# Optimization experiments

Measured on AMD Instinct MI355X. Metric: run time of the kernel, lower is better.

## Reference

```python
import jax, jax.numpy as jnp
import numpy as np

N_NODES = 50000
N_EDGES = 800000
NFEAT = 256
NHID = 128
NCLASS = 40
NLAYERS = 3


def setup_inputs() -> dict:
    key = jax.random.key(0)
    ks = jax.random.split(key, 8)
    x = jax.random.normal(ks[0], (N_NODES, NFEAT), dtype=jnp.float32)
    edge_src = jax.random.randint(ks[1], (N_EDGES,), 0, N_NODES, dtype=jnp.int32)
    edge_dst = jax.random.randint(ks[2], (N_EDGES,), 0, N_NODES, dtype=jnp.int32)
    # Kaiming-ish scaled params
    W_in = jax.random.normal(ks[3], (NFEAT, NHID), dtype=jnp.float32) / np.sqrt(NFEAT)
    b_in = jnp.zeros((NHID,), dtype=jnp.float32)
    W_mlps = jax.random.normal(ks[4], (NLAYERS, NHID, NHID), dtype=jnp.float32) / np.sqrt(NHID)
    b_mlps = jnp.zeros((NLAYERS, NHID), dtype=jnp.float32)
    W_out = jax.random.normal(ks[5], (NHID, NCLASS), dtype=jnp.float32) / np.sqrt(NHID)
    b_out = jnp.zeros((NCLASS,), dtype=jnp.float32)
    return {"x": x, "edge_src": edge_src, "edge_dst": edge_dst,
            "W_in": W_in, "b_in": b_in, "W_mlps": W_mlps, "b_mlps": b_mlps,
            "W_out": W_out, "b_out": b_out}


def reference(x, edge_src, edge_dst, W_in, b_in, W_mlps, b_mlps, W_out, b_out):
    # Dropout is identity in eval mode (training=False).
    n = x.shape[0]
    h = jax.nn.relu(x @ W_in + b_in)                       # [N, H]
    for i in range(NLAYERS):
        # GINConv with eps=0: h' = h + sum_{(s->d) in E} h[s] scattered to d
        agg = jax.ops.segment_sum(h[edge_src], edge_dst, num_segments=n)
        h = jax.nn.relu((h + agg) @ W_mlps[i] + b_mlps[i])  # [N, H]
    logits = h @ W_out + b_out                              # [N, C]
    return jax.nn.log_softmax(logits, axis=1)
```

## Files before the change

kernel.cpp:

```cpp
#include <hip/hip_runtime.h>
#include <math.h>

#define NHID 128
#define NFEAT 256
#define NCLASS 40

typedef __bf16 bf16x8 __attribute__((ext_vector_type(8)));
typedef __bf16 bf16x4 __attribute__((ext_vector_type(4)));
typedef float floatx4 __attribute__((ext_vector_type(4)));


__global__ __launch_bounds__(256) void bucket_hist(const int* __restrict__ edst,
                                                   int* __restrict__ bucket_counts,
                                                   int E, int nbuck) {
    __shared__ int lh[256];
    int tid = threadIdx.x;
    lh[tid] = 0;
    __syncthreads();
    int base = blockIdx.x * 4096;
#pragma unroll
    for (int k = 0; k < 16; ++k) {
        int e = base + k * 256 + tid;
        if (e < E) atomicAdd(&lh[edst[e] >> 8], 1);
    }
    __syncthreads();
    if (tid < nbuck && lh[tid]) atomicAdd(&bucket_counts[tid], lh[tid]);
}

__global__ __launch_bounds__(256) void bucket_scan(const int* __restrict__ counts,
                                                   int* __restrict__ start,
                                                   int* __restrict__ cursor,
                                                   int* __restrict__ row_ptr,
                                                   int nbuck, int E, int N) {
    __shared__ int lds[256];
    int tid = threadIdx.x;
    int v = (tid < nbuck) ? counts[tid] : 0;
    lds[tid] = v;
    __syncthreads();
    for (int off = 1; off < 256; off <<= 1) {
        int t = (tid >= off) ? lds[tid - off] : 0;
        __syncthreads();
        lds[tid] += t;
        __syncthreads();
    }
    int excl = lds[tid] - v;
    if (tid < nbuck) { start[tid] = excl; cursor[tid] = excl; }
    if (tid == 0) { start[nbuck] = E; row_ptr[N] = E; }
}

__global__ __launch_bounds__(256) void bucket_scatter(const int* __restrict__ esrc,
                                                      const int* __restrict__ edst,
                                                      int* __restrict__ cursor,
                                                      unsigned int* __restrict__ bdata,
                                                      int E, int nbuck) {
    __shared__ int lh[256];
    __shared__ int lbase[256];
    int tid = threadIdx.x;
    lh[tid] = 0;
    __syncthreads();
    int base = blockIdx.x * 4096;
    unsigned int recs[16];
    short bks[16];
    short lofs[16];
#pragma unroll
    for (int k = 0; k < 16; ++k) {
        int e = base + k * 256 + tid;
        bks[k] = -1;
        if (e < E) {
            int d = edst[e];
            int s = esrc[e];
            int b = d >> 8;
            recs[k] = ((unsigned int)(d & 255) << 16) | (unsigned int)s;
            bks[k] = (short)b;
            lofs[k] = (short)atomicAdd(&lh[b], 1);
        }
    }
    __syncthreads();
    if (tid < nbuck && lh[tid]) lbase[tid] = atomicAdd(&cursor[tid], lh[tid]);
    __syncthreads();
#pragma unroll
    for (int k = 0; k < 16; ++k) {
        if (bks[k] >= 0) bdata[lbase[bks[k]] + lofs[k]] = recs[k];
    }
}

__global__ __launch_bounds__(256) void bucket_finalize(const unsigned int* __restrict__ bdata,
                                                       const int* __restrict__ start,
                                                       int* __restrict__ row_ptr,
                                                       int* __restrict__ srcs,
                                                       int N) {
    __shared__ int hist[256];
    __shared__ int cur[256];
    int b = blockIdx.x;
    int tid = threadIdx.x;
    int s0 = start[b];
    int cnt = start[b + 1] - s0;
    hist[tid] = 0;
    __syncthreads();
    for (int i = tid; i < cnt; i += 256) atomicAdd(&hist[bdata[s0 + i] >> 16], 1);
    __syncthreads();
    int v0 = hist[tid];
    __syncthreads();
    for (int off = 1; off < 256; off <<= 1) {
        int t = (tid >= off) ? hist[tid - off] : 0;
        __syncthreads();
        hist[tid] += t;
        __syncthreads();
    }
    int excl = hist[tid] - v0;
    cur[tid] = excl;
    int node = b * 256 + tid;
    if (node < N) row_ptr[node] = s0 + excl;
    __syncthreads();
    for (int i = tid; i < cnt; i += 256) {
        unsigned int r = bdata[s0 + i];
        int p = atomicAdd(&cur[r >> 16], 1);
        srcs[s0 + p] = (int)(r & 0xffffu);
    }
}

template <int K>
__global__ __launch_bounds__(256) void transpose_split(const float* __restrict__ src,
                                                       __bf16* __restrict__ dhi,
                                                       __bf16* __restrict__ dlo, int total) {
    int i = blockIdx.x * 256 + threadIdx.x;
    if (i >= total) return;
    int per = 128 * K;
    int l = i / per;
    int r = i - l * per;
    int n = r / K;
    int k = r - n * K;
    float v = src[(size_t)l * per + (size_t)k * 128 + n];
    __bf16 hi = (__bf16)v;
    dhi[i] = hi;
    dlo[i] = (__bf16)(v - (float)hi);
}

__global__ __launch_bounds__(256) void aggregate_fused(const __bf16* __restrict__ hhi,
                                                       const __bf16* __restrict__ hlo,
                                                       const int* __restrict__ row_ptr,
                                                       const int* __restrict__ srcs,
                                                       __bf16* __restrict__ ohi,
                                                       __bf16* __restrict__ olo, int N) {
    int tid = threadIdx.x;
    int node = blockIdx.x * 4 + (tid >> 6);
    if (node >= N) return;
    int lane = tid & 63;
    int g = lane >> 4;
    int c = lane & 15;
    int beg = row_ptr[node];
    int end = row_ptr[node + 1];
    const bf16x8* hv = (const bf16x8*)hhi;

    float a[8], b2[8];
#pragma unroll
    for (int j = 0; j < 8; ++j) { a[j] = 0.f; b2[j] = 0.f; }

    int i = beg;
    for (; i + 8 <= end; i += 8) {
        int s0 = srcs[i + g];
        int s1 = srcs[i + 4 + g];
        bf16x8 v0 = hv[(size_t)s0 * 16 + c];
        bf16x8 v1 = hv[(size_t)s1 * 16 + c];
#pragma unroll
        for (int j = 0; j < 8; ++j) { a[j] += (float)v0[j]; b2[j] += (float)v1[j]; }
    }
    for (; i < end; i += 4) {
        if (i + g < end) {
            int s = srcs[i + g];
            bf16x8 v = hv[(size_t)s * 16 + c];
#pragma unroll
            for (int j = 0; j < 8; ++j) a[j] += (float)v[j];
        }
    }
#pragma unroll
    for (int j = 0; j < 8; ++j) a[j] += b2[j];
#pragma unroll
    for (int j = 0; j < 8; ++j) a[j] += __shfl_xor(a[j], 16);
#pragma unroll
    for (int j = 0; j < 8; ++j) a[j] += __shfl_xor(a[j], 32);

    if (g == 0) {
        bf16x8 sh = ((const bf16x8*)hhi)[(size_t)node * 16 + c];
        bf16x8 sl = ((const bf16x8*)hlo)[(size_t)node * 16 + c];
        bf16x8 whi, wlo;
#pragma unroll
        for (int j = 0; j < 8; ++j) {
            float v = a[j] + (float)sh[j] + (float)sl[j];
            __bf16 h = (__bf16)v;
            whi[j] = h;
            wlo[j] = (__bf16)(v - (float)h);
        }
        ((bf16x8*)ohi)[(size_t)node * 16 + c] = whi;
        ((bf16x8*)olo)[(size_t)node * 16 + c] = wlo;
    }
}

template <int MODE>
__global__ __launch_bounds__(256) void gemm_mfma(
    const float* __restrict__ Af, const __bf16* __restrict__ Ahi,
    const __bf16* __restrict__ Alo,
    const __bf16* __restrict__ Wthi, const __bf16* __restrict__ Wtlo,
    const float* __restrict__ bias, __bf16* __restrict__ Ohi,
    __bf16* __restrict__ Olo, int M, int K) {
    __shared__ __align__(16) char smem[49152];
    __bf16* sAhi = (__bf16*)smem;
    __bf16* sAlo = (__bf16*)(smem + 8192);
    __bf16* sWhi = (__bf16*)(smem + 16384);
    __bf16* sWlo = (__bf16*)(smem + 32768);

    int tid = threadIdx.x;
    int row0 = blockIdx.x * 64;
    int wave = tid >> 6;
    int l = tid & 63;
    int m16 = l & 15;
    int q = l >> 4;
    int axor = m16 & 7;
    int arow = wave * 16 + m16;

    floatx4 acc[8];
#pragma unroll
    for (int t = 0; t < 8; ++t) acc[t] = (floatx4){0.f, 0.f, 0.f, 0.f};

    for (int k0 = 0; k0 < K; k0 += 64) {
#pragma unroll
        for (int it = 0; it < 2; ++it) {
            int lin = it * 2048 + tid * 8;
            int row = lin >> 6, k = lin & 63;
            int g = min(row0 + row, M - 1);
            int off = row * 64 + (((k >> 3) ^ (row & 7)) << 3);
            if (MODE == 0) {
                float4 v0 = *(const float4*)&Af[(size_t)g * K + k0 + k];
                float4 v1 = *(const float4*)&Af[(size_t)g * K + k0 + k + 4];
                float s[8] = {v0.x, v0.y, v0.z, v0.w, v1.x, v1.y, v1.z, v1.w};
                bf16x8 shi, slo;
#pragma unroll
                for (int j = 0; j < 8; ++j) {
                    __bf16 h = (__bf16)s[j];
                    shi[j] = h;
                    slo[j] = (__bf16)(s[j] - (float)h);
                }
                *(bf16x8*)(sAhi + off) = shi;
                *(bf16x8*)(sAlo + off) = slo;
            } else {
                *(bf16x8*)(sAhi + off) = *(const bf16x8*)&Ahi[(size_t)g * 128 + k0 + k];
                *(bf16x8*)(sAlo + off) = *(const bf16x8*)&Alo[(size_t)g * 128 + k0 + k];
            }
        }
#pragma unroll
        for (int it = 0; it < 4; ++it) {
            int lin = it * 2048 + tid * 8;
            int n = lin >> 6, kk = lin & 63;
            int off = n * 64 + (((kk >> 3) ^ (n & 7)) << 3);
            *(bf16x8*)(sWhi + off) = *(const bf16x8*)&Wthi[(size_t)n * K + k0 + kk];
            *(bf16x8*)(sWlo + off) = *(const bf16x8*)&Wtlo[(size_t)n * K + k0 + kk];
        }
        __syncthreads();

#pragma unroll
        for (int s = 0; s < 2; ++s) {
            int sw = (((s * 4 + q) ^ axor) << 3);
            bf16x8 ahi = *(bf16x8*)(sAhi + arow * 64 + sw);
            bf16x8 alo = *(bf16x8*)(sAlo + arow * 64 + sw);
#pragma unroll
            for (int t = 0; t < 8; ++t) {
                int n = t * 16 + m16;
                bf16x8 bhi = *(bf16x8*)(sWhi + n * 64 + sw);
                bf16x8 blo = *(bf16x8*)(sWlo + n * 64 + sw);
                acc[t] = __builtin_amdgcn_mfma_f32_16x16x32_bf16(ahi, bhi, acc[t], 0, 0, 0);
                acc[t] = __builtin_amdgcn_mfma_f32_16x16x32_bf16(alo, bhi, acc[t], 0, 0, 0);
                acc[t] = __builtin_amdgcn_mfma_f32_16x16x32_bf16(ahi, blo, acc[t], 0, 0, 0);
            }
        }
        __syncthreads();
    }

    float* eps = (float*)(smem + 16384);
#pragma unroll
    for (int t = 0; t < 8; ++t) {
        int col = t * 16 + m16;
        float bb = bias[col];
#pragma unroll
        for (int i = 0; i < 4; ++i) {
            int row = wave * 16 + q * 4 + i;
            eps[row * 128 + col] = fmaxf(acc[t][i] + bb, 0.f);
        }
    }
    __syncthreads();
#pragma unroll
    for (int it = 0; it < 8; ++it) {
        int lin = it * 1024 + tid * 4;
        int row = lin >> 7, col = lin & 127;
        int g = row0 + row;
        if (g < M) {
            float4 v = *(float4*)(eps + lin);
            bf16x4 hi, lo;
            float vv[4] = {v.x, v.y, v.z, v.w};
#pragma unroll
            for (int j = 0; j < 4; ++j) {
                __bf16 h = (__bf16)vv[j];
                hi[j] = h;
                lo[j] = (__bf16)(vv[j] - (float)h);
            }
            *(bf16x4*)&Ohi[(size_t)g * 128 + col] = hi;
            *(bf16x4*)&Olo[(size_t)g * 128 + col] = lo;
        }
    }
}

__global__ __launch_bounds__(256) void out_logsoftmax(const __bf16* __restrict__ hhi,
                                                      const __bf16* __restrict__ hlo,
                                                      const float* __restrict__ Wout,
                                                      const float* __restrict__ bout,
                                                      float* __restrict__ out, int M) {
    __shared__ float sW[128 * NCLASS];
    __shared__ float sb[NCLASS];
    __shared__ float sH[32 * 132];
    int tid = threadIdx.x;
    for (int i = tid; i < 128 * NCLASS; i += 256) sW[i] = Wout[i];
    if (tid < NCLASS) sb[tid] = bout[tid];
    int row0 = blockIdx.x * 32;
#pragma unroll
    for (int it = 0; it < 4; ++it) {
        int i = tid * 4 + it * 1024;
        int r = i >> 7, k = i & 127;
        int rr = min(row0 + r, M - 1);
        uint2 uh = *(const uint2*)&hhi[(size_t)rr * 128 + k];
        uint2 ul = *(const uint2*)&hlo[(size_t)rr * 128 + k];
        sH[r * 132 + k + 0] = __uint_as_float(uh.x << 16) + __uint_as_float(ul.x << 16);
        sH[r * 132 + k + 1] = __uint_as_float(uh.x & 0xffff0000u) + __uint_as_float(ul.x & 0xffff0000u);
        sH[r * 132 + k + 2] = __uint_as_float(uh.y << 16) + __uint_as_float(ul.y << 16);
        sH[r * 132 + k + 3] = __uint_as_float(uh.y & 0xffff0000u) + __uint_as_float(ul.y & 0xffff0000u);
    }
    __syncthreads();

    int r = tid >> 3;
    int cg = tid & 7;
    float z[5];
#pragma unroll
    for (int j = 0; j < 5; ++j) z[j] = sb[cg * 5 + j];
    for (int k = 0; k < 128; ++k) {
        float a = sH[r * 132 + k];
#pragma unroll
        for (int j = 0; j < 5; ++j) z[j] += a * sW[k * NCLASS + cg * 5 + j];
    }
    float m = z[0];
#pragma unroll
    for (int j = 1; j < 5; ++j) m = fmaxf(m, z[j]);
    for (int off = 1; off < 8; off <<= 1) m = fmaxf(m, __shfl_xor(m, off));
    float s = 0.f;
#pragma unroll
    for (int j = 0; j < 5; ++j) s += expf(z[j] - m);
    for (int off = 1; off < 8; off <<= 1) s += __shfl_xor(s, off);
    float lse = m + logf(s);
    int row = row0 + r;
    if (row < M) {
#pragma unroll
        for (int j = 0; j < 5; ++j) out[(size_t)row * NCLASS + cg * 5 + j] = z[j] - lse;
    }
}

extern "C" void kernel_launch(void* const* d_in, const int* in_sizes, int n_in,
                              void* d_out, int out_size, void* d_ws, size_t ws_size,
                              hipStream_t stream) {
    const float* x      = (const float*)d_in[0];
    const int*   esrc   = (const int*)d_in[1];
    const int*   edst   = (const int*)d_in[2];
    const float* W_in   = (const float*)d_in[3];
    const float* b_in   = (const float*)d_in[4];
    const float* W_mlps = (const float*)d_in[5];
    const float* b_mlps = (const float*)d_in[6];
    const float* W_out  = (const float*)d_in[7];
    const float* b_out  = (const float*)d_in[8];
    float* out = (float*)d_out;

    int N = in_sizes[0] / NFEAT;
    int E = in_sizes[1];
    int nbuck = (N + 255) >> 8;

    char* ws = (char*)d_ws;
    size_t hb = (((size_t)N * NHID * sizeof(__bf16)) + 255) & ~(size_t)255;
    __bf16* h_hi_a = (__bf16*)ws;
    __bf16* h_lo_a = (__bf16*)(ws + hb);
    __bf16* h_hi_b = (__bf16*)(ws + 2 * hb);
    __bf16* h_lo_b = (__bf16*)(ws + 3 * hb);
    __bf16* sum_hi = (__bf16*)(ws + 4 * hb);
    __bf16* sum_lo = (__bf16*)(ws + 5 * hb);
    unsigned int* bdata = (unsigned int*)(ws + 4 * hb);
    char* ip = ws + 6 * hb;
    int* row_ptr = (int*)ip;  ip += (((size_t)(N + 1) * 4) + 255) & ~(size_t)255;
    int* srcs    = (int*)ip;  ip += (((size_t)E * 4) + 255) & ~(size_t)255;
    int* bucket_counts = (int*)ip;  ip += 1024;
    int* bucket_start  = (int*)ip;  ip += 1024;
    int* bucket_cursor = (int*)ip;  ip += 1024;
    __bf16* Wt_in_hi   = (__bf16*)ip;  ip += 128 * NFEAT * 2;
    __bf16* Wt_in_lo   = (__bf16*)ip;  ip += 128 * NFEAT * 2;
    __bf16* Wt_mlps_hi = (__bf16*)ip;  ip += 3 * 128 * NHID * 2;
    __bf16* Wt_mlps_lo = (__bf16*)ip;  ip += 3 * 128 * NHID * 2;

    int eb4 = (E + 4095) / 4096;

    hipMemsetAsync(bucket_counts, 0, 1024, stream);
    bucket_hist<<<eb4, 256, 0, stream>>>(edst, bucket_counts, E, nbuck);
    bucket_scan<<<1, 256, 0, stream>>>(bucket_counts, bucket_start, bucket_cursor,
                                       row_ptr, nbuck, E, N);
    bucket_scatter<<<eb4, 256, 0, stream>>>(esrc, edst, bucket_cursor, bdata, E, nbuck);
    bucket_finalize<<<nbuck, 256, 0, stream>>>(bdata, bucket_start, row_ptr, srcs, N);

    transpose_split<NFEAT><<<(128 * NFEAT + 255) / 256, 256, 0, stream>>>(
        W_in, Wt_in_hi, Wt_in_lo, 128 * NFEAT);
    transpose_split<NHID><<<(3 * 128 * NHID + 255) / 256, 256, 0, stream>>>(
        W_mlps, Wt_mlps_hi, Wt_mlps_lo, 3 * 128 * NHID);

    int gb = (N + 63) / 64;
    gemm_mfma<0><<<gb, 256, 0, stream>>>(x, (const __bf16*)nullptr, (const __bf16*)nullptr,
                                         Wt_in_hi, Wt_in_lo, b_in, h_hi_a, h_lo_a, N, NFEAT);

    __bf16* cur_hi = h_hi_a; __bf16* cur_lo = h_lo_a;
    __bf16* nxt_hi = h_hi_b; __bf16* nxt_lo = h_lo_b;
    for (int i = 0; i < 3; ++i) {
        aggregate_fused<<<(N + 3) / 4, 256, 0, stream>>>(cur_hi, cur_lo, row_ptr, srcs,
                                                         sum_hi, sum_lo, N);
        gemm_mfma<1><<<gb, 256, 0, stream>>>(
            (const float*)nullptr, sum_hi, sum_lo,
            Wt_mlps_hi + (size_t)i * 128 * NHID, Wt_mlps_lo + (size_t)i * 128 * NHID,
            b_mlps + (size_t)i * NHID, nxt_hi, nxt_lo, N, NHID);
        __bf16* t;
        t = cur_hi; cur_hi = nxt_hi; nxt_hi = t;
        t = cur_lo; cur_lo = nxt_lo; nxt_lo = t;
    }

    out_logsoftmax<<<(N + 31) / 32, 256, 0, stream>>>(cur_hi, cur_lo, W_out, b_out, out, N);
}
```

Before: 327.9 us.

## Split hidden features into quarter-planes for cache-friendly neighbour aggregation

The GEMM epilogue and the output kernel now store and read hidden activations in four column-quarter planes of 32 features each. Aggregation walks one quarter at a time over a contiguous node range per block, so the gathered working set per pass is a quarter of the full feature matrix and is more likely to stay in cache. The aggregate kernel also changes to a persistent grid of 1024 blocks with 16 nodes per wave and 4 lanes per node, and uses non-temporal loads and stores. Costs are that the edge list and row pointers are read four times, lanes are less parallel per node, and the aggregate output stays row-major while the GEMM reads it as before.

```diff
diff --git a/kernel.cpp b/kernel.cpp
--- a/kernel.cpp
+++ b/kernel.cpp
@@ -136,63 +136,71 @@
     dlo[i] = (__bf16)(v - (float)hi);
 }
 
-__global__ __launch_bounds__(256) void aggregate_fused(const __bf16* __restrict__ hhi,
-                                                       const __bf16* __restrict__ hlo,
-                                                       const int* __restrict__ row_ptr,
-                                                       const int* __restrict__ srcs,
-                                                       __bf16* __restrict__ ohi,
-                                                       __bf16* __restrict__ olo, int N) {
-    int tid = threadIdx.x;
-    int node = blockIdx.x * 4 + (tid >> 6);
-    if (node >= N) return;
+__global__ __launch_bounds__(256) void aggregate_q(const __bf16* __restrict__ hhi,
+                                                   const __bf16* __restrict__ hlo,
+                                                   const int* __restrict__ row_ptr,
+                                                   const int* __restrict__ srcs,
+                                                   __bf16* __restrict__ ohi,
+                                                   __bf16* __restrict__ olo, int N) {
+    int tid = threadIdx.x;
+    int wave = tid >> 6;
     int lane = tid & 63;
-    int g = lane >> 4;
-    int c = lane & 15;
-    int beg = row_ptr[node];
-    int end = row_ptr[node + 1];
-    const bf16x8* hv = (const bf16x8*)hhi;
-
-    float a[8], b2[8];
-#pragma unroll
-    for (int j = 0; j < 8; ++j) { a[j] = 0.f; b2[j] = 0.f; }
-
-    int i = beg;
-    for (; i + 8 <= end; i += 8) {
-        int s0 = srcs[i + g];
-        int s1 = srcs[i + 4 + g];
-        bf16x8 v0 = hv[(size_t)s0 * 16 + c];
-        bf16x8 v1 = hv[(size_t)s1 * 16 + c];
-#pragma unroll
-        for (int j = 0; j < 8; ++j) { a[j] += (float)v0[j]; b2[j] += (float)v1[j]; }
-    }
-    for (; i < end; i += 4) {
-        if (i + g < end) {
-            int s = srcs[i + g];
-            bf16x8 v = hv[(size_t)s * 16 + c];
-#pragma unroll
-            for (int j = 0; j < 8; ++j) a[j] += (float)v[j];
-        }
-    }
-#pragma unroll
-    for (int j = 0; j < 8; ++j) a[j] += b2[j];
-#pragma unroll
-    for (int j = 0; j < 8; ++j) a[j] += __shfl_xor(a[j], 16);
-#pragma unroll
-    for (int j = 0; j < 8; ++j) a[j] += __shfl_xor(a[j], 32);
-
-    if (g == 0) {
-        bf16x8 sh = ((const bf16x8*)hhi)[(size_t)node * 16 + c];
-        bf16x8 sl = ((const bf16x8*)hlo)[(size_t)node * 16 + c];
-        bf16x8 whi, wlo;
-#pragma unroll
-        for (int j = 0; j < 8; ++j) {
-            float v = a[j] + (float)sh[j] + (float)sl[j];
-            __bf16 h = (__bf16)v;
-            whi[j] = h;
-            wlo[j] = (__bf16)(v - (float)h);
-        }
-        ((bf16x8*)ohi)[(size_t)node * 16 + c] = whi;
-        ((bf16x8*)olo)[(size_t)node * 16 + c] = wlo;
+    int nsub = lane >> 2;
+    int c = lane & 3;
+    int per = (N + (int)gridDim.x - 1) / (int)gridDim.x;
+    int nb = (int)blockIdx.x * per;
+    int ne = nb + per;
+    if (ne > N) ne = N;
+    size_t qstride = (size_t)N * 32;
+    for (int q = 0; q < 4; ++q) {
+        const bf16x8* hq = (const bf16x8*)(hhi + (size_t)q * qstride);
+        const bf16x8* lq = (const bf16x8*)(hlo + (size_t)q * qstride);
+        for (int n0 = nb + wave * 16; n0 < ne; n0 += 64) {
+            int node = n0 + nsub;
+            bool valid = node < ne;
+            int beg = 0, end = 0;
+            if (valid) {
+                beg = row_ptr[node];
+                end = row_ptr[node + 1];
+            }
+            float a[8];
+#pragma unroll
+            for (int j = 0; j < 8; ++j) a[j] = 0.f;
+            int i = beg;
+            for (; i + 4 <= end; i += 4) {
+                int s0 = __builtin_nontemporal_load(&srcs[i]);
+                int s1 = __builtin_nontemporal_load(&srcs[i + 1]);
+                int s2 = __builtin_nontemporal_load(&srcs[i + 2]);
+                int s3 = __builtin_nontemporal_load(&srcs[i + 3]);
+                bf16x8 v0 = hq[(size_t)s0 * 4 + c];
+                bf16x8 v1 = hq[(size_t)s1 * 4 + c];
+                bf16x8 v2 = hq[(size_t)s2 * 4 + c];
+                bf16x8 v3 = hq[(size_t)s3 * 4 + c];
+#pragma unroll
+                for (int j = 0; j < 8; ++j)
+                    a[j] += ((float)v0[j] + (float)v1[j]) + ((float)v2[j] + (float)v3[j]);
+            }
+            for (; i < end; ++i) {
+                int s = __builtin_nontemporal_load(&srcs[i]);
+                bf16x8 v = hq[(size_t)s * 4 + c];
+#pragma unroll
+                for (int j = 0; j < 8; ++j) a[j] += (float)v[j];
+            }
+            if (valid) {
+                bf16x8 sh = hq[(size_t)node * 4 + c];
+                bf16x8 sl = __builtin_nontemporal_load(&lq[(size_t)node * 4 + c]);
+                bf16x8 whi, wlo;
+#pragma unroll
+                for (int j = 0; j < 8; ++j) {
+                    float v = a[j] + (float)sh[j] + (float)sl[j];
+                    __bf16 h = (__bf16)v;
+                    whi[j] = h;
+                    wlo[j] = (__bf16)(v - (float)h);
+                }
+                __builtin_nontemporal_store(whi, &((bf16x8*)ohi)[(size_t)node * 16 + q * 4 + c]);
+                __builtin_nontemporal_store(wlo, &((bf16x8*)olo)[(size_t)node * 16 + q * 4 + c]);
+            }
+        }
     }
 }
 
@@ -287,6 +295,7 @@
         }
     }
     __syncthreads();
+    size_t qs = (size_t)M * 32;
 #pragma unroll
     for (int it = 0; it < 8; ++it) {
         int lin = it * 1024 + tid * 4;
@@ -302,8 +311,9 @@
                 hi[j] = h;
                 lo[j] = (__bf16)(vv[j] - (float)h);
             }
-            *(bf16x4*)&Ohi[(size_t)g * 128 + col] = hi;
-            *(bf16x4*)&Olo[(size_t)g * 128 + col] = lo;
+            size_t qoff = (size_t)(col >> 5) * qs + (size_t)g * 32 + (col & 31);
+            *(bf16x4*)&Ohi[qoff] = hi;
+            *(bf16x4*)&Olo[qoff] = lo;
         }
     }
 }
@@ -320,13 +330,15 @@
     for (int i = tid; i < 128 * NCLASS; i += 256) sW[i] = Wout[i];
     if (tid < NCLASS) sb[tid] = bout[tid];
     int row0 = blockIdx.x * 32;
+    size_t qs = (size_t)M * 32;
 #pragma unroll
     for (int it = 0; it < 4; ++it) {
         int i = tid * 4 + it * 1024;
         int r = i >> 7, k = i & 127;
         int rr = min(row0 + r, M - 1);
-        uint2 uh = *(const uint2*)&hhi[(size_t)rr * 128 + k];
-        uint2 ul = *(const uint2*)&hlo[(size_t)rr * 128 + k];
+        size_t qoff = (size_t)(k >> 5) * qs + (size_t)rr * 32 + (k & 31);
+        uint2 uh = *(const uint2*)&hhi[qoff];
+        uint2 ul = *(const uint2*)&hlo[qoff];
         sH[r * 132 + k + 0] = __uint_as_float(uh.x << 16) + __uint_as_float(ul.x << 16);
         sH[r * 132 + k + 1] = __uint_as_float(uh.x & 0xffff0000u) + __uint_as_float(ul.x & 0xffff0000u);
         sH[r * 132 + k + 2] = __uint_as_float(uh.y << 16) + __uint_as_float(ul.y << 16);
@@ -419,8 +431,8 @@
     __bf16* cur_hi = h_hi_a; __bf16* cur_lo = h_lo_a;
     __bf16* nxt_hi = h_hi_b; __bf16* nxt_lo = h_lo_b;
     for (int i = 0; i < 3; ++i) {
-        aggregate_fused<<<(N + 3) / 4, 256, 0, stream>>>(cur_hi, cur_lo, row_ptr, srcs,
-                                                         sum_hi, sum_lo, N);
+        aggregate_q<<<1024, 256, 0, stream>>>(cur_hi, cur_lo, row_ptr, srcs,
+                                              sum_hi, sum_lo, N);
         gemm_mfma<1><<<gb, 256, 0, stream>>>(
             (const float*)nullptr, sum_hi, sum_lo,
             Wt_mlps_hi + (size_t)i * 128 * NHID, Wt_mlps_lo + (size_t)i * 128 * NHID,
```

Result: slower. 416.6 us (+27.0%).
